# Performance work log

Hardware: AMD Instinct MI355X
Metric: run time of the kernel (lower is better)

The kernel has to match this reference:

```python
import jax, jax.numpy as jnp
import numpy as np

N_VARS = 100000
N_CLAUSES = 400000
NNZ = 1200000
D = 128
EPSILON = 1e-6


def setup_inputs() -> dict:
    key = jax.random.key(0)
    k1, k2, k3 = jax.random.split(key, 3)
    variables = jax.random.normal(k1, (N_VARS, D), dtype=jnp.float32)
    adj_vals = jnp.ones((NNZ,), dtype=jnp.float32)  # SAT adjacency is binary
    adj_rows = jax.random.randint(k2, (NNZ,), 0, N_CLAUSES, dtype=jnp.int32)  # clause ids
    adj_cols = jax.random.randint(k3, (NNZ,), 0, 2 * N_VARS, dtype=jnp.int32)  # literal ids
    return {"variables": variables, "adj_vals": adj_vals, "adj_rows": adj_rows, "adj_cols": adj_cols}


def reference(variables, adj_vals, adj_rows, adj_cols):
    n_vars, d = variables.shape
    # literals = [vars; vars], append a ones column to count clause degree alongside features
    literals = jnp.concatenate([variables, variables], axis=0)  # [2V, d]
    lit1 = jnp.concatenate([literals, jnp.ones((2 * n_vars, 1), literals.dtype)], axis=1)  # [2V, d+1]
    # clauses_val = adj @ lit1  (sparse COO -> gather + segment_sum over clause ids)
    msgs = lit1[adj_cols] * adj_vals[:, None]  # [nnz, d+1]
    clauses_val = jax.ops.segment_sum(msgs, adj_rows, num_segments=N_CLAUSES)  # [C, d+1]
    # lit_new = adj^T @ clauses_val  (gather clause values, scatter-add to literals)
    back = clauses_val[adj_rows] * adj_vals[:, None]  # [nnz, d+1]
    lit_new = jax.ops.segment_sum(back, adj_cols, num_segments=2 * n_vars)  # [2V, d+1]
    lit_a, lit_b = jnp.split(lit_new, 2, axis=0)
    var_new_deg = lit_a + lit_b  # [V, d+1]
    var_new = var_new_deg[:, :-1]
    deg = var_new_deg[:, -1:]
    mean = var_new / jnp.maximum(deg, 2.0)
    v = variables - mean
    variance = jnp.mean(jnp.square(v), axis=1, keepdims=True)
    return v * jax.lax.rsqrt(variance + EPSILON)
```

## Files before the change

kernel.cpp:

```cpp
#include <hip/hip_runtime.h>

#define D_C 128
#define EPS 1e-6f
#define NCONST 400000

#define P1B    512
#define PREPB  512
#define P1CAP  40
#define SH_C   11
#define SH_V   9
#define BINS_C 196
#define BINS_V 196
#define KC     2048
#define KV     512
#define CCAP   16
#define VCAP   32
#define P1TOT  ((size_t)P1B * BINS_C * P1CAP)

static __device__ __forceinline__ unsigned short f2bf(float f) {
    unsigned u = __float_as_uint(f);
    return (unsigned short)((u + 0x7FFFu + ((u >> 16) & 1u)) >> 16);
}


__global__ void __launch_bounds__(256)
pass1_fused(const int* __restrict__ rows, const int* __restrict__ cols,
            const float* __restrict__ vals,
            const float* __restrict__ vars, unsigned short* __restrict__ vb,
            int do_prep,
            uint2* __restrict__ c_p, int* __restrict__ scnt_c,
            uint2* __restrict__ v_p, int* __restrict__ scnt_v,
            int nnz, int n_vars) {
    __shared__ int cur[BINS_C + BINS_V];
    if (blockIdx.x >= P1B) {
        if (!do_prep) return;
        int n4 = n_vars * (D_C / 4);
        int stride = (gridDim.x - P1B) * 256;
        for (int i = (blockIdx.x - P1B) * 256 + threadIdx.x; i < n4; i += stride) {
            const float4 x = ((const float4*)vars)[i];
            ushort4 o;
            o.x = f2bf(x.x); o.y = f2bf(x.y); o.z = f2bf(x.z); o.w = f2bf(x.w);
            ((ushort4*)vb)[i] = o;
        }
        return;
    }

    for (int i = threadIdx.x; i < BINS_C + BINS_V; i += 256) cur[i] = 0;
    __syncthreads();

    int stride = P1B * 256;
    for (int e = blockIdx.x * 256 + threadIdx.x; e < nnz; e += stride) {
        int r = rows[e];
        int c = cols[e];
        unsigned u = __float_as_uint(vals[e]);
        int vv = (c >= n_vars) ? (c - n_vars) : c;

        int b = r >> SH_C;
        int slot = atomicAdd(&cur[b], 1);
        if (slot < P1CAP) {
            uint2 pk;
            pk.x = (u & 0xFFFE0000u) | (unsigned)vv;
            pk.y = (unsigned)(r & (KC - 1));
            c_p[((size_t)blockIdx.x * BINS_C + b) * P1CAP + slot] = pk;
        }

        int b2 = vv >> SH_V;
        int slot2 = atomicAdd(&cur[BINS_C + b2], 1);
        if (slot2 < P1CAP) {
            uint2 pk;
            pk.x = (u & 0xFFF80000u) | (unsigned)r;
            pk.y = (unsigned)(vv & (KV - 1));
            v_p[((size_t)blockIdx.x * BINS_V + b2) * P1CAP + slot2] = pk;
        }
    }
    __syncthreads();
    for (int i = threadIdx.x; i < BINS_C; i += 256) {
        int v = cur[i];
        scnt_c[blockIdx.x * BINS_C + i] = v > P1CAP ? P1CAP : v;
    }
    for (int i = threadIdx.x; i < BINS_V; i += 256) {
        int v = cur[BINS_C + i];
        scnt_v[blockIdx.x * BINS_V + i] = v > P1CAP ? P1CAP : v;
    }
}

__global__ void __launch_bounds__(1024)
pass2_place(const uint2* __restrict__ c_p, const int* __restrict__ scnt_c,
            const uint2* __restrict__ v_p, const int* __restrict__ scnt_v,
            int* __restrict__ cbuf, int* __restrict__ ccnt,
            int* __restrict__ vbuf, int* __restrict__ vcnt) {
    __shared__ int cur[KC];
    bool cl = blockIdx.x < BINS_C;
    int bin = cl ? blockIdx.x : blockIdx.x - BINS_C;
    int K   = cl ? KC : KV;
    int CAP = cl ? CCAP : VCAP;
    for (int i = threadIdx.x; i < K; i += 1024) cur[i] = 0;
    __syncthreads();

    const uint2* P  = cl ? c_p : v_p;
    const int* SC   = cl ? scnt_c : scnt_v;
    int* buf        = cl ? cbuf : vbuf;

    int wid = threadIdx.x >> 6, lane = threadIdx.x & 63;
    for (int p1 = wid; p1 < P1B; p1 += 16) {
        int cell = p1 * BINS_C + bin;
        int cnt = SC[cell];
        uint2 pk = make_uint2(0u, 0u);
        if (lane < P1CAP) pk = P[(size_t)cell * P1CAP + lane];
        if (lane < cnt) {
            int k = (int)pk.y;
            int slot = atomicAdd(&cur[k], 1);
            if (slot < CAP) buf[((size_t)bin * K + k) * CAP + slot] = (int)pk.x;
        }
    }
    __syncthreads();
    int* cntarr = cl ? ccnt : vcnt;
    for (int i = threadIdx.x; i < K; i += 1024)
        cntarr[(size_t)bin * K + i] = cur[i];
}

__global__ void __launch_bounds__(256)
clause_q(const unsigned short* __restrict__ vb,
         const int* __restrict__ ccnt, const int* __restrict__ cbuf,
         unsigned short* __restrict__ cmat, float* __restrict__ cdegp,
         int n_clauses) {
    int tid = blockIdx.x * 256 + threadIdx.x;
    int clause = tid >> 4;
    int l = tid & 15;
    if (clause >= n_clauses) return;

    int cnt = ccnt[clause];
    cnt = cnt > CCAP ? CCAP : cnt;

    int myvv = 0; float myval = 0.0f;
    if (l < cnt) {
        unsigned entry = (unsigned)cbuf[(size_t)clause * CCAP + l];
        myvv  = (int)(entry & 0x1FFFFu);
        myval = __uint_as_float(entry & 0xFFFE0000u);
    }

    float a0=0,a1=0,a2=0,a3=0,a4=0,a5=0,a6=0,a7=0, cd=0;
    for (int j = 0; j < cnt; j++) {
        int vv = __shfl(myvv, j, 16);
        float v1 = __shfl(myval, j, 16);
        const uint4 x = *(const uint4*)(vb + (size_t)vv * D_C + l * 8);
        a0 = fmaf(v1, __uint_as_float(x.x << 16), a0);
        a1 = fmaf(v1, __uint_as_float(x.x & 0xFFFF0000u), a1);
        a2 = fmaf(v1, __uint_as_float(x.y << 16), a2);
        a3 = fmaf(v1, __uint_as_float(x.y & 0xFFFF0000u), a3);
        a4 = fmaf(v1, __uint_as_float(x.z << 16), a4);
        a5 = fmaf(v1, __uint_as_float(x.z & 0xFFFF0000u), a5);
        a6 = fmaf(v1, __uint_as_float(x.w << 16), a6);
        a7 = fmaf(v1, __uint_as_float(x.w & 0xFFFF0000u), a7);
        cd += v1;
    }

    uint4 o;
    o.x = (unsigned)f2bf(a0) | ((unsigned)f2bf(a1) << 16);
    o.y = (unsigned)f2bf(a2) | ((unsigned)f2bf(a3) << 16);
    o.z = (unsigned)f2bf(a4) | ((unsigned)f2bf(a5) << 16);
    o.w = (unsigned)f2bf(a6) | ((unsigned)f2bf(a7) << 16);
    *(uint4*)(cmat + (size_t)clause * D_C + l * 8) = o;
    if (l == 0) cdegp[clause] = cd;
}

__global__ void __launch_bounds__(256)
var_q(const float* __restrict__ vars,
      const int* __restrict__ vcnt, const int* __restrict__ vbuf,
      const unsigned short* __restrict__ cmat, const float* __restrict__ cdegp,
      float* __restrict__ out, int n_vars) {
    int tid = blockIdx.x * 256 + threadIdx.x;
    int v = tid >> 4;
    int l = tid & 15;
    if (v >= n_vars) return;

    int cnt = vcnt[v];
    cnt = cnt > VCAP ? VCAP : cnt;

    int r0 = 0, r1 = 0; float val0 = 0, val1 = 0, cdg0 = 0, cdg1 = 0;
    if (l < cnt) {
        unsigned e = (unsigned)vbuf[(size_t)v * VCAP + l];
        r0   = (int)(e & 0x7FFFFu);
        val0 = __uint_as_float(e & 0xFFF80000u);
        cdg0 = cdegp[r0];
    }
    if (l + 16 < cnt) {
        unsigned e = (unsigned)vbuf[(size_t)v * VCAP + 16 + l];
        r1   = (int)(e & 0x7FFFFu);
        val1 = __uint_as_float(e & 0xFFF80000u);
        cdg1 = cdegp[r1];
    }

    float a0=0,a1=0,a2=0,a3=0,a4=0,a5=0,a6=0,a7=0, dg=0;
    int cmain = cnt < 16 ? cnt : 16;
    for (int j = 0; j < cmain; j++) {
        int r = __shfl(r0, j, 16);
        float v2 = __shfl(val0, j, 16);
        float cdg = __shfl(cdg0, j, 16);
        const uint4 p = *(const uint4*)(cmat + (size_t)r * D_C + l * 8);
        a0 = fmaf(v2, __uint_as_float(p.x << 16), a0);
        a1 = fmaf(v2, __uint_as_float(p.x & 0xFFFF0000u), a1);
        a2 = fmaf(v2, __uint_as_float(p.y << 16), a2);
        a3 = fmaf(v2, __uint_as_float(p.y & 0xFFFF0000u), a3);
        a4 = fmaf(v2, __uint_as_float(p.z << 16), a4);
        a5 = fmaf(v2, __uint_as_float(p.z & 0xFFFF0000u), a5);
        a6 = fmaf(v2, __uint_as_float(p.w << 16), a6);
        a7 = fmaf(v2, __uint_as_float(p.w & 0xFFFF0000u), a7);
        dg = fmaf(v2, cdg, dg);
    }
    for (int j = 16; j < cnt; j++) {
        int r = __shfl(r1, j - 16, 16);
        float v2 = __shfl(val1, j - 16, 16);
        float cdg = __shfl(cdg1, j - 16, 16);
        const uint4 p = *(const uint4*)(cmat + (size_t)r * D_C + l * 8);
        a0 = fmaf(v2, __uint_as_float(p.x << 16), a0);
        a1 = fmaf(v2, __uint_as_float(p.x & 0xFFFF0000u), a1);
        a2 = fmaf(v2, __uint_as_float(p.y << 16), a2);
        a3 = fmaf(v2, __uint_as_float(p.y & 0xFFFF0000u), a3);
        a4 = fmaf(v2, __uint_as_float(p.z << 16), a4);
        a5 = fmaf(v2, __uint_as_float(p.z & 0xFFFF0000u), a5);
        a6 = fmaf(v2, __uint_as_float(p.w << 16), a6);
        a7 = fmaf(v2, __uint_as_float(p.w & 0xFFFF0000u), a7);
        dg = fmaf(v2, cdg, dg);
    }

    float inv = 1.0f / fmaxf(dg, 2.0f);
    const float4 m0 = *(const float4*)(vars + (size_t)v * D_C + l * 8);
    const float4 m1 = *(const float4*)(vars + (size_t)v * D_C + l * 8 + 4);
    float w0 = m0.x - a0 * inv;
    float w1 = m0.y - a1 * inv;
    float w2 = m0.z - a2 * inv;
    float w3 = m0.w - a3 * inv;
    float w4 = m1.x - a4 * inv;
    float w5 = m1.y - a5 * inv;
    float w6 = m1.z - a6 * inv;
    float w7 = m1.w - a7 * inv;

    float ss = w0*w0 + w1*w1 + w2*w2 + w3*w3 + w4*w4 + w5*w5 + w6*w6 + w7*w7;
    #pragma unroll
    for (int off = 8; off > 0; off >>= 1)
        ss += __shfl_xor(ss, off, 16);
    float scale = rsqrtf(ss * (1.0f / (float)D_C) + EPS);

    float4 o0, o1;
    o0.x = w0 * scale; o0.y = w1 * scale; o0.z = w2 * scale; o0.w = w3 * scale;
    o1.x = w4 * scale; o1.y = w5 * scale; o1.z = w6 * scale; o1.w = w7 * scale;
    *(float4*)(out + (size_t)v * D_C + l * 8) = o0;
    *(float4*)(out + (size_t)v * D_C + l * 8 + 4) = o1;
}

__global__ void __launch_bounds__(256)
clause_half_f32(const float* __restrict__ vars,
                const int* __restrict__ ccnt, const int* __restrict__ cbuf,
                unsigned short* __restrict__ cmat, float* __restrict__ cdegp,
                int n_clauses) {
    int wave = (blockIdx.x * blockDim.x + threadIdx.x) >> 6;
    int lane = threadIdx.x & 63;
    if (wave >= n_clauses) return;
    int l = lane & 31, h = lane >> 5;

    int cnt = ccnt[wave];
    cnt = cnt > CCAP ? CCAP : cnt;

    int myvv = 0; float myval = 0.0f;
    if (lane < cnt) {
        unsigned entry = (unsigned)cbuf[(size_t)wave * CCAP + lane];
        myvv  = (int)(entry & 0x1FFFFu);
        myval = __uint_as_float(entry & 0xFFFE0000u);
    }

    float a0 = 0, a1 = 0, a2 = 0, a3 = 0, cd = 0;
    for (int i = 0; i < cnt; i += 2) {
        int j = i + h;
        int vv = __shfl(myvv, j, 64);
        float v1 = (j < cnt) ? __shfl(myval, j, 64) : 0.0f;
        const float4 x = *(const float4*)(vars + (size_t)vv * D_C + l * 4);
        a0 = fmaf(v1, x.x, a0);
        a1 = fmaf(v1, x.y, a1);
        a2 = fmaf(v1, x.z, a2);
        a3 = fmaf(v1, x.w, a3);
        cd += v1;
    }
    a0 += __shfl_xor(a0, 32, 64);
    a1 += __shfl_xor(a1, 32, 64);
    a2 += __shfl_xor(a2, 32, 64);
    a3 += __shfl_xor(a3, 32, 64);
    cd += __shfl_xor(cd, 32, 64);

    if (h == 0) {
        ushort4 o;
        o.x = f2bf(a0); o.y = f2bf(a1); o.z = f2bf(a2); o.w = f2bf(a3);
        *(ushort4*)(cmat + (size_t)wave * D_C + l * 4) = o;
    }
    if (lane == 0) cdegp[wave] = cd;
}


__global__ void hist_kernel(const int* __restrict__ rows, const int* __restrict__ cols,
                            int* __restrict__ cnt, int nnz, int n_vars) {
    int e = blockIdx.x * blockDim.x + threadIdx.x;
    if (e >= nnz) return;
    atomicAdd(&cnt[rows[e]], 1);
    int c = cols[e];
    int v = (c >= n_vars) ? (c - n_vars) : c;
    atomicAdd(&cnt[NCONST + v], 1);
}

__global__ void scan_partial(const int* __restrict__ cnt, int* __restrict__ bsum, int L) {
    __shared__ int sm[256];
    int t = threadIdx.x;
    int i0 = blockIdx.x * 1024 + t * 4;
    int s = 0;
    #pragma unroll
    for (int k = 0; k < 4; k++) { int i = i0 + k; if (i < L) s += cnt[i]; }
    sm[t] = s; __syncthreads();
    for (int off = 128; off > 0; off >>= 1) {
        if (t < off) sm[t] += sm[t + off];
        __syncthreads();
    }
    if (t == 0) bsum[blockIdx.x] = sm[0];
}

__global__ void scan_bsums(int* __restrict__ bsum, int nb) {
    __shared__ int sm[512];
    int t = threadIdx.x;
    int x = (t < nb) ? bsum[t] : 0;
    sm[t] = x; __syncthreads();
    for (int off = 1; off < 512; off <<= 1) {
        int y = (t >= off) ? sm[t - off] : 0;
        __syncthreads();
        sm[t] += y;
        __syncthreads();
    }
    if (t < nb) bsum[t] = sm[t] - x;
}

__global__ void scan_final(int* __restrict__ cnt_cursor, int* __restrict__ basep,
                           const int* __restrict__ bsum, int L) {
    __shared__ int sm[256];
    int t = threadIdx.x;
    int i0 = blockIdx.x * 1024 + t * 4;
    int c[4]; int tot = 0;
    #pragma unroll
    for (int k = 0; k < 4; k++) { int i = i0 + k; c[k] = (i < L) ? cnt_cursor[i] : 0; tot += c[k]; }
    sm[t] = tot; __syncthreads();
    for (int off = 1; off < 256; off <<= 1) {
        int y = (t >= off) ? sm[t - off] : 0;
        __syncthreads();
        sm[t] += y;
        __syncthreads();
    }
    int run = sm[t] - tot + bsum[blockIdx.x];
    #pragma unroll
    for (int k = 0; k < 4; k++) {
        int i = i0 + k;
        if (i < L) {
            basep[i] = run;
            cnt_cursor[i] = run;
            run += c[k];
            if (i == L - 1) basep[L] = run;
        }
    }
}

__global__ void scatter_kernel(const int* __restrict__ rows, const int* __restrict__ cols,
                               int* __restrict__ cursor, int* __restrict__ eid,
                               int nnz, int n_vars) {
    int e = blockIdx.x * blockDim.x + threadIdx.x;
    if (e >= nnz) return;
    int p = atomicAdd(&cursor[rows[e]], 1);
    eid[p] = e;
    int c = cols[e];
    int v = (c >= n_vars) ? (c - n_vars) : c;
    int p2 = atomicAdd(&cursor[NCONST + v], 1);
    eid[p2] = e;
}

__global__ void __launch_bounds__(256)
clause_kernel(const float* __restrict__ vars, const float* __restrict__ vals,
              const int* __restrict__ cols,
              const int* __restrict__ base, const int* __restrict__ eid,
              unsigned* __restrict__ cmat, float* __restrict__ cdegp,
              int n_vars, int n_clauses) {
    int wave = (blockIdx.x * blockDim.x + threadIdx.x) >> 6;
    int lane = threadIdx.x & 63;
    if (wave >= n_clauses) return;
    int j0 = base[wave], j1 = base[wave + 1];
    int d = j1 - j0;

    int mycol = 0; float myval = 0.0f;
    if (lane < d) { int e = eid[j0 + lane]; mycol = cols[e]; myval = vals[e]; }

    float csx = 0.0f, csy = 0.0f, cd = 0.0f;
    int dmain = d > 64 ? 64 : d;
    for (int i = 0; i < dmain; i++) {
        int c = __shfl(mycol, i, 64);
        float v1 = __shfl(myval, i, 64);
        int vv = (c >= n_vars) ? (c - n_vars) : c;
        const float2 x = *(const float2*)(vars + (size_t)vv * D_C + lane * 2);
        csx = fmaf(v1, x.x, csx);
        csy = fmaf(v1, x.y, csy);
        cd += v1;
    }
    for (int j = j0 + 64; j < j1; j++) {
        int e = eid[j]; int c = cols[e]; float v1 = vals[e];
        int vv = (c >= n_vars) ? (c - n_vars) : c;
        const float2 x = *(const float2*)(vars + (size_t)vv * D_C + lane * 2);
        csx = fmaf(v1, x.x, csx);
        csy = fmaf(v1, x.y, csy);
        cd += v1;
    }

    unsigned p = ((unsigned)f2bf(csy) << 16) | (unsigned)f2bf(csx);
    cmat[(size_t)wave * 64 + lane] = p;
    if (lane == 0) cdegp[wave] = cd;
}

__global__ void __launch_bounds__(256)
var_kernel(const float* __restrict__ vars, const float* __restrict__ vals,
           const int* __restrict__ rows,
           const int* __restrict__ base, const int* __restrict__ eid,
           const unsigned* __restrict__ cmat, const float* __restrict__ cdegp,
           float* __restrict__ out, int n_vars) {
    int wave = (blockIdx.x * blockDim.x + threadIdx.x) >> 6;
    int lane = threadIdx.x & 63;
    if (wave >= n_vars) return;
    int j0 = base[NCONST + wave], j1 = base[NCONST + wave + 1];
    int d = j1 - j0;

    int myr = 0; float myval = 0.0f;
    if (lane < d) { int e = eid[j0 + lane]; myr = rows[e]; myval = vals[e]; }

    float ax = 0.0f, ay = 0.0f, dg = 0.0f;
    int dmain = d > 64 ? 64 : d;
    for (int i = 0; i < dmain; i++) {
        int r = __shfl(myr, i, 64);
        float v2 = __shfl(myval, i, 64);
        unsigned p = cmat[(size_t)r * 64 + lane];
        float cx = __uint_as_float(p << 16);
        float cy = __uint_as_float(p & 0xFFFF0000u);
        ax = fmaf(v2, cx, ax);
        ay = fmaf(v2, cy, ay);
        dg = fmaf(v2, cdegp[r], dg);
    }
    for (int j = j0 + 64; j < j1; j++) {
        int e = eid[j]; int r = rows[e]; float v2 = vals[e];
        unsigned p = cmat[(size_t)r * 64 + lane];
        float cx = __uint_as_float(p << 16);
        float cy = __uint_as_float(p & 0xFFFF0000u);
        ax = fmaf(v2, cx, ax);
        ay = fmaf(v2, cy, ay);
        dg = fmaf(v2, cdegp[r], dg);
    }

    float inv = 1.0f / fmaxf(dg, 2.0f);
    const float2 mv = *(const float2*)(vars + (size_t)wave * D_C + lane * 2);
    float vx = mv.x - ax * inv;
    float vy = mv.y - ay * inv;

    float ss = vx * vx + vy * vy;
    #pragma unroll
    for (int off = 32; off > 0; off >>= 1)
        ss += __shfl_xor(ss, off, 64);
    float scale = rsqrtf(ss * (1.0f / (float)D_C) + EPS);

    float2 o;
    o.x = vx * scale;
    o.y = vy * scale;
    *(float2*)(out + (size_t)wave * D_C + lane * 2) = o;
}


extern "C" void kernel_launch(void* const* d_in, const int* in_sizes, int n_in,
                              void* d_out, int out_size, void* d_ws, size_t ws_size,
                              hipStream_t stream) {
    const float* vars = (const float*)d_in[0];
    const float* vals = (const float*)d_in[1];
    const int*   rows = (const int*)d_in[2];
    const int*   cols = (const int*)d_in[3];
    float* out = (float*)d_out;

    const int nnz    = in_sizes[1];
    const int n_vars = in_sizes[0] / D_C;
    const int NC     = NCONST;
    const int t = 256;

    size_t base_fast = (size_t)NC * D_C * 2 + (size_t)NC * 4 +
                       (size_t)BINS_C * KC * 4 + (size_t)BINS_V * KV * 4 +
                       (size_t)BINS_C * KC * CCAP * 4 + (size_t)BINS_V * KV * VCAP * 4;
    size_t need_vb = base_fast + (size_t)n_vars * D_C * 2;

    if (ws_size >= base_fast && n_vars == 100000) {
        unsigned short* cmat = (unsigned short*)d_ws;
        uint2* c_p  = (uint2*)d_ws;
        uint2* v_p  = c_p + P1TOT;
        int* scnt_c = (int*)(v_p + P1TOT);
        int* scnt_v = scnt_c + P1B * BINS_C;
        float* cdegp = (float*)((char*)d_ws + (size_t)NC * D_C * 2);
        int* ccnt    = (int*)(cdegp + NC);
        int* vcnt    = ccnt + (size_t)BINS_C * KC;
        int* cbuf    = vcnt + (size_t)BINS_V * KV;
        int* vbuf    = cbuf + (size_t)BINS_C * KC * CCAP;
        unsigned short* vb = (unsigned short*)(vbuf + (size_t)BINS_V * KV * VCAP);

        bool use_vb = (ws_size >= need_vb);
        int p1grid = use_vb ? (P1B + PREPB) : P1B;

        pass1_fused<<<p1grid, 256, 0, stream>>>(rows, cols, vals, vars, vb,
                                                use_vb ? 1 : 0,
                                                c_p, scnt_c, v_p, scnt_v,
                                                nnz, n_vars);
        pass2_place<<<BINS_C + BINS_V, 1024, 0, stream>>>(
            c_p, scnt_c, v_p, scnt_v, cbuf, ccnt, vbuf, vcnt);
        if (use_vb) {
            clause_q<<<(NC * 16 + t - 1) / t, t, 0, stream>>>(
                vb, ccnt, cbuf, cmat, cdegp, NC);
        } else {
            clause_half_f32<<<(NC * 64 + t - 1) / t, t, 0, stream>>>(
                vars, ccnt, cbuf, cmat, cdegp, NC);
        }
        var_q<<<(n_vars * 16 + t - 1) / t, t, 0, stream>>>(
            vars, vcnt, vbuf, cmat, cdegp, out, n_vars);
    } else {
        const int L  = NC + n_vars;
        const int nb = (L + 1023) / 1024;

        unsigned* cmatw = (unsigned*)d_ws;
        float* cdegp   = (float*)(cmatw + (size_t)NC * 64);
        int* base      = (int*)(cdegp + NC);
        int* cursor    = base + (L + 1);
        int* bsum      = cursor + L;
        int* eid       = bsum + 512;

        hipMemsetAsync(cursor, 0, (size_t)L * sizeof(int), stream);

        hist_kernel<<<(nnz + t - 1) / t, t, 0, stream>>>(rows, cols, cursor, nnz, n_vars);
        scan_partial<<<nb, 256, 0, stream>>>(cursor, bsum, L);
        scan_bsums<<<1, 512, 0, stream>>>(bsum, nb);
        scan_final<<<nb, 256, 0, stream>>>(cursor, base, bsum, L);
        scatter_kernel<<<(nnz + t - 1) / t, t, 0, stream>>>(rows, cols, cursor, eid, nnz, n_vars);

        clause_kernel<<<(NC * 64 + t - 1) / t, t, 0, stream>>>(
            vars, vals, cols, base, eid, cmatw, cdegp, n_vars, NC);
        var_kernel<<<(n_vars * 64 + t - 1) / t, t, 0, stream>>>(
            vars, vals, rows, base, eid, cmatw, cdegp, out, n_vars);
    }
}
```

Baseline: 340.4 us.

## Replace two-pass binned bucketing with direct global-atomic scatter into adjacency buffers

The old two-kernel local-bin partition (shared-memory binning into per-block staging, then a placement pass) is replaced by a single scatter kernel. It uses global atomicAdd on per-clause and per-variable counters to write packed entries straight into cbuf/vbuf, after a memset of the counter arrays. This removes one kernel launch and the staging-buffer round trip, but relies on scattered global atomics and non-coalesced writes across the whole counter array. Slot order within each row now depends on atomic timing, and the old per-bin P1CAP overflow truncation is gone.

```diff
diff --git a/kernel.cpp b/kernel.cpp
--- a/kernel.cpp
+++ b/kernel.cpp
@@ -4,18 +4,14 @@
 #define EPS 1e-6f
 #define NCONST 400000
 
-#define P1B    512
-#define PREPB  512
-#define P1CAP  40
-#define SH_C   11
-#define SH_V   9
+#define SCB    1024
+#define PREPB  1024
 #define BINS_C 196
 #define BINS_V 196
 #define KC     2048
 #define KV     512
 #define CCAP   16
 #define VCAP   32
-#define P1TOT  ((size_t)P1B * BINS_C * P1CAP)
 
 static __device__ __forceinline__ unsigned short f2bf(float f) {
     unsigned u = __float_as_uint(f);
@@ -24,19 +20,18 @@
 
 
 __global__ void __launch_bounds__(256)
-pass1_fused(const int* __restrict__ rows, const int* __restrict__ cols,
-            const float* __restrict__ vals,
-            const float* __restrict__ vars, unsigned short* __restrict__ vb,
-            int do_prep,
-            uint2* __restrict__ c_p, int* __restrict__ scnt_c,
-            uint2* __restrict__ v_p, int* __restrict__ scnt_v,
-            int nnz, int n_vars) {
-    __shared__ int cur[BINS_C + BINS_V];
-    if (blockIdx.x >= P1B) {
+scatter_prep(const int* __restrict__ rows, const int* __restrict__ cols,
+             const float* __restrict__ vals,
+             const float* __restrict__ vars, unsigned short* __restrict__ vb,
+             int do_prep,
+             int* __restrict__ ccnt, int* __restrict__ cbuf,
+             int* __restrict__ vcnt, int* __restrict__ vbuf,
+             int nnz, int n_vars) {
+    if (blockIdx.x >= SCB) {
         if (!do_prep) return;
         int n4 = n_vars * (D_C / 4);
-        int stride = (gridDim.x - P1B) * 256;
-        for (int i = (blockIdx.x - P1B) * 256 + threadIdx.x; i < n4; i += stride) {
+        int stride = (gridDim.x - SCB) * 256;
+        for (int i = (blockIdx.x - SCB) * 256 + threadIdx.x; i < n4; i += stride) {
             const float4 x = ((const float4*)vars)[i];
             ushort4 o;
             o.x = f2bf(x.x); o.y = f2bf(x.y); o.z = f2bf(x.z); o.w = f2bf(x.w);
@@ -45,78 +40,21 @@
         return;
     }
 
-    for (int i = threadIdx.x; i < BINS_C + BINS_V; i += 256) cur[i] = 0;
-    __syncthreads();
-
-    int stride = P1B * 256;
+    int stride = SCB * 256;
     for (int e = blockIdx.x * 256 + threadIdx.x; e < nnz; e += stride) {
         int r = rows[e];
         int c = cols[e];
         unsigned u = __float_as_uint(vals[e]);
         int vv = (c >= n_vars) ? (c - n_vars) : c;
 
-        int b = r >> SH_C;
-        int slot = atomicAdd(&cur[b], 1);
-        if (slot < P1CAP) {
-            uint2 pk;
-            pk.x = (u & 0xFFFE0000u) | (unsigned)vv;
-            pk.y = (unsigned)(r & (KC - 1));
-            c_p[((size_t)blockIdx.x * BINS_C + b) * P1CAP + slot] = pk;
-        }
-
-        int b2 = vv >> SH_V;
-        int slot2 = atomicAdd(&cur[BINS_C + b2], 1);
-        if (slot2 < P1CAP) {
-            uint2 pk;
-            pk.x = (u & 0xFFF80000u) | (unsigned)r;
-            pk.y = (unsigned)(vv & (KV - 1));
-            v_p[((size_t)blockIdx.x * BINS_V + b2) * P1CAP + slot2] = pk;
-        }
-    }
-    __syncthreads();
-    for (int i = threadIdx.x; i < BINS_C; i += 256) {
-        int v = cur[i];
-        scnt_c[blockIdx.x * BINS_C + i] = v > P1CAP ? P1CAP : v;
-    }
-    for (int i = threadIdx.x; i < BINS_V; i += 256) {
-        int v = cur[BINS_C + i];
-        scnt_v[blockIdx.x * BINS_V + i] = v > P1CAP ? P1CAP : v;
-    }
-}
-
-__global__ void __launch_bounds__(1024)
-pass2_place(const uint2* __restrict__ c_p, const int* __restrict__ scnt_c,
-            const uint2* __restrict__ v_p, const int* __restrict__ scnt_v,
-            int* __restrict__ cbuf, int* __restrict__ ccnt,
-            int* __restrict__ vbuf, int* __restrict__ vcnt) {
-    __shared__ int cur[KC];
-    bool cl = blockIdx.x < BINS_C;
-    int bin = cl ? blockIdx.x : blockIdx.x - BINS_C;
-    int K   = cl ? KC : KV;
-    int CAP = cl ? CCAP : VCAP;
-    for (int i = threadIdx.x; i < K; i += 1024) cur[i] = 0;
-    __syncthreads();
-
-    const uint2* P  = cl ? c_p : v_p;
-    const int* SC   = cl ? scnt_c : scnt_v;
-    int* buf        = cl ? cbuf : vbuf;
-
-    int wid = threadIdx.x >> 6, lane = threadIdx.x & 63;
-    for (int p1 = wid; p1 < P1B; p1 += 16) {
-        int cell = p1 * BINS_C + bin;
-        int cnt = SC[cell];
-        uint2 pk = make_uint2(0u, 0u);
-        if (lane < P1CAP) pk = P[(size_t)cell * P1CAP + lane];
-        if (lane < cnt) {
-            int k = (int)pk.y;
-            int slot = atomicAdd(&cur[k], 1);
-            if (slot < CAP) buf[((size_t)bin * K + k) * CAP + slot] = (int)pk.x;
-        }
-    }
-    __syncthreads();
-    int* cntarr = cl ? ccnt : vcnt;
-    for (int i = threadIdx.x; i < K; i += 1024)
-        cntarr[(size_t)bin * K + i] = cur[i];
+        int slot = atomicAdd(&ccnt[r], 1);
+        if (slot < CCAP)
+            cbuf[(size_t)r * CCAP + slot] = (int)((u & 0xFFFE0000u) | (unsigned)vv);
+
+        int slot2 = atomicAdd(&vcnt[vv], 1);
+        if (slot2 < VCAP)
+            vbuf[(size_t)vv * VCAP + slot2] = (int)((u & 0xFFF80000u) | (unsigned)r);
+    }
 }
 
 __global__ void __launch_bounds__(256)
@@ -492,10 +430,6 @@
 
     if (ws_size >= base_fast && n_vars == 100000) {
         unsigned short* cmat = (unsigned short*)d_ws;
-        uint2* c_p  = (uint2*)d_ws;
-        uint2* v_p  = c_p + P1TOT;
-        int* scnt_c = (int*)(v_p + P1TOT);
-        int* scnt_v = scnt_c + P1B * BINS_C;
         float* cdegp = (float*)((char*)d_ws + (size_t)NC * D_C * 2);
         int* ccnt    = (int*)(cdegp + NC);
         int* vcnt    = ccnt + (size_t)BINS_C * KC;
@@ -504,14 +438,16 @@
         unsigned short* vb = (unsigned short*)(vbuf + (size_t)BINS_V * KV * VCAP);
 
         bool use_vb = (ws_size >= need_vb);
-        int p1grid = use_vb ? (P1B + PREPB) : P1B;
-
-        pass1_fused<<<p1grid, 256, 0, stream>>>(rows, cols, vals, vars, vb,
-                                                use_vb ? 1 : 0,
-                                                c_p, scnt_c, v_p, scnt_v,
-                                                nnz, n_vars);
-        pass2_place<<<BINS_C + BINS_V, 1024, 0, stream>>>(
-            c_p, scnt_c, v_p, scnt_v, cbuf, ccnt, vbuf, vcnt);
+        int p1grid = use_vb ? (SCB + PREPB) : SCB;
+
+        hipMemsetAsync(ccnt, 0,
+                       ((size_t)BINS_C * KC + (size_t)BINS_V * KV) * sizeof(int),
+                       stream);
+
+        scatter_prep<<<p1grid, 256, 0, stream>>>(rows, cols, vals, vars, vb,
+                                                 use_vb ? 1 : 0,
+                                                 ccnt, cbuf, vcnt, vbuf,
+                                                 nnz, n_vars);
         if (use_vb) {
             clause_q<<<(NC * 16 + t - 1) / t, t, 0, stream>>>(
                 vb, ccnt, cbuf, cmat, cdegp, NC);
```

Result: slower. 395.7 us (+16.3%).
